# Optimization experiments

Measured on AMD Instinct MI355X. Metric: run time of the kernel, lower is better.

The kernel has to match this reference:

```python
import jax, jax.numpy as jnp
import numpy as np

N_NODES = 100000


def setup_inputs() -> dict:
    key = jax.random.key(0)
    k1, k2, k3 = jax.random.split(key, 3)
    X = jax.random.normal(k1, (N_NODES, 128), dtype=jnp.float32)
    W = jax.random.normal(k2, (128, 128), dtype=jnp.float32) * (1.0 / np.sqrt(128))
    edge_index = jax.random.randint(k3, (2, 1600000), 0, N_NODES, dtype=jnp.int64)
    return {"X": X, "W": W, "edge_index": edge_index}


def reference(X, W, edge_index):
    # GCNConv: out = D_hat^{-1/2} (A + I) D_hat^{-1/2} @ (X W^T)
    N = X.shape[0]
    row, col = edge_index[0], edge_index[1]
    # A_hat = A + I : append self-loop edges
    loops = jnp.arange(N, dtype=row.dtype)
    row_h = jnp.concatenate([row, loops])
    col_h = jnp.concatenate([col, loops])
    # D_hat = A_hat.sum(0): column sums -> degree indexed by col
    deg = jax.ops.segment_sum(jnp.ones(col_h.shape[0], dtype=X.dtype), col_h,
                              num_segments=N)
    d_invsqrt = deg ** -0.5  # deg >= 1 due to self loops
    # edge value of H = D^-1/2 A_hat D^-1/2
    val = d_invsqrt[row_h] * d_invsqrt[col_h]  # [E+N]
    # linear projection (nn.Linear, no bias): X @ W^T
    X_hat = X @ W.T  # [N, out]
    # SpMM (sum): out[r] += val * X_hat[c]
    msgs = val[:, None] * X_hat[col_h]  # [E+N, out]
    return jax.ops.segment_sum(msgs, row_h, num_segments=N)
```

## Files before the change

kernel.cpp:

```cpp
#include <hip/hip_runtime.h>
#include <hip/hip_bf16.h>
#include <stdint.h>

typedef __bf16 bf16_t;
typedef bf16_t bf16x8 __attribute__((ext_vector_type(8)));
typedef bf16_t bf16x2 __attribute__((ext_vector_type(2)));
typedef float  f32x4  __attribute__((ext_vector_type(4)));
typedef float  f32x2  __attribute__((ext_vector_type(2)));

#define N_FEAT 128
#define NBMAX  196
#define BINB   512

__global__ void detect_k(const int* __restrict__ edges, int* __restrict__ flag) {
    int v = edges[2 * threadIdx.x + 1];
    unsigned long long m = __ballot(v != 0);
    if (threadIdx.x == 0) *flag = (m == 0ull) ? 1 : 0;
}
__device__ inline int eread(const int* __restrict__ edges, int f, long i) {
    return f ? edges[2 * i] : edges[i];
}

__device__ inline bf16x8 cvt8(const float* __restrict__ p) {
    f32x4 lo = *(const f32x4*)p;
    f32x4 hi = *(const f32x4*)(p + 4);
    bf16x8 r;
    r[0] = (bf16_t)lo[0]; r[1] = (bf16_t)lo[1]; r[2] = (bf16_t)lo[2]; r[3] = (bf16_t)lo[3];
    r[4] = (bf16_t)hi[0]; r[5] = (bf16_t)hi[1]; r[6] = (bf16_t)hi[2]; r[7] = (bf16_t)hi[3];
    return r;
}

__device__ inline int block_scan_incl(int v, int* wsum ) {
    const int t = threadIdx.x, lane = t & 63, wid = t >> 6;
    int x = v;
#pragma unroll
    for (int off = 1; off < 64; off <<= 1) {
        int y = __shfl_up(x, off);
        if (lane >= off) x += y;
    }
    if (lane == 63) wsum[wid] = x;
    __syncthreads();
    int add = 0;
    for (int w = 0; w < wid; ++w) add += wsum[w];
    return x + add;
}

__global__ __launch_bounds__(256) void wconv_k(const float* __restrict__ W,
                                               bf16_t* __restrict__ Wbf) {
    int i = blockIdx.x * 256 + threadIdx.x;
    Wbf[i] = (bf16_t)W[i];
}

__global__ __launch_bounds__(64) void gemm_xwt2(const float* __restrict__ X,
                                                const bf16_t* __restrict__ Wbf,
                                                bf16_t* __restrict__ Xhat) {
    const int lane = threadIdx.x;
    const int m  = lane & 15;
    const int kq = lane >> 4;
    const long r0 = (long)blockIdx.x * 16;

    f32x4 acc[8];
#pragma unroll
    for (int c = 0; c < 8; ++c) acc[c] = (f32x4){0.f, 0.f, 0.f, 0.f};

    const float* xrow = X + (r0 + m) * N_FEAT + kq * 8;
#pragma unroll
    for (int kb = 0; kb < 4; ++kb) {
        bf16x8 a = cvt8(xrow + kb * 32);
#pragma unroll
        for (int c = 0; c < 8; ++c) {
            bf16x8 b = *(const bf16x8*)(Wbf + (c * 16 + m) * N_FEAT + kb * 32 + kq * 8);
            acc[c] = __builtin_amdgcn_mfma_f32_16x16x32_bf16(a, b, acc[c], 0, 0, 0);
        }
    }
#pragma unroll
    for (int c = 0; c < 8; ++c) {
#pragma unroll
        for (int i = 0; i < 4; ++i) {
            long r = r0 + kq * 4 + i;
            Xhat[r * N_FEAT + c * 16 + m] = (bf16_t)acc[c][i];
        }
    }
}


__global__ __launch_bounds__(256) void bin_k(const int* __restrict__ edges,
                                             const int* __restrict__ flag,
                                             int E, int N, int NB,
                                             int* __restrict__ hist) {
    __shared__ int h[2 * NBMAX];
    const int blk = blockIdx.x;
    const int nb2 = 2 * NB;
    for (int j = threadIdx.x; j < nb2; j += 256) h[j] = 0;
    __syncthreads();
    const int f = *flag;
    const int chunk = (E + BINB - 1) / BINB;
    const int e0 = blk * chunk, e1 = min(E, e0 + chunk);
    for (int e = e0 + (int)threadIdx.x; e < e1; e += 256) {
        int r = eread(edges, f, e);
        int c = eread(edges, f, (long)E + e);
        if ((unsigned)r < (unsigned)N && (unsigned)c < (unsigned)N) {
            atomicAdd(&h[r >> 9], 1);
            atomicAdd(&h[NB + (c >> 9)], 1);
        }
    }
    __syncthreads();
    for (int j = threadIdx.x; j < nb2; j += 256) hist[(long)j * BINB + blk] = h[j];
}

__global__ __launch_bounds__(BINB) void scan_k(const int* __restrict__ hist, int NB,
                                               int* __restrict__ baseTab,
                                               int* __restrict__ totals) {
    __shared__ int wsum[BINB / 64];
    const int j = blockIdx.x;
    const int t = threadIdx.x;
    int v = hist[(long)j * BINB + t];
    int incl = block_scan_incl(v, wsum);
    baseTab[(long)j * BINB + t] = incl - v;
    if (t == BINB - 1) totals[j] = incl;
}

__global__ __launch_bounds__(512) void bucketbase_k(const int* __restrict__ totals,
                                                    int NB, int N,
                                                    int* __restrict__ famBase,
                                                    int* __restrict__ start) {
    __shared__ int wsum[8];
    __shared__ int sh_tot0;
    const int t = threadIdx.x;
    const int nb2 = 2 * NB;
    int v = (t < nb2) ? totals[t] : 0;
    int incl = block_scan_incl(v, wsum);
    int excl = incl - v;
    if (t == NB) sh_tot0 = excl;
    __syncthreads();
    if (t < NB) famBase[t] = excl;
    if (t == NB) { famBase[NB] = excl; start[N] = excl; }
    if (t >= NB && t < nb2) famBase[NB + 1 + (t - NB)] = excl - sh_tot0;
    if (t == nb2 - 1) famBase[NB + 1 + NB] = incl - sh_tot0;
}

__global__ __launch_bounds__(256) void bscatter_k(const int* __restrict__ edges,
                                                  const int* __restrict__ flag,
                                                  int E, int N, int NB,
                                                  const int* __restrict__ baseTab,
                                                  const int* __restrict__ famBase,
                                                  unsigned* __restrict__ rowbuf,
                                                  int* __restrict__ colbuf) {
    __shared__ int cur[2 * NBMAX];
    const int blk = blockIdx.x;
    const int nb2 = 2 * NB;
    for (int j = threadIdx.x; j < nb2; j += 256) {
        int fb = (j < NB) ? famBase[j] : famBase[NB + 1 + (j - NB)];
        cur[j] = fb + baseTab[(long)j * BINB + blk];
    }
    __syncthreads();
    const int f = *flag;
    const int chunk = (E + BINB - 1) / BINB;
    const int e0 = blk * chunk, e1 = min(E, e0 + chunk);
    for (int e = e0 + (int)threadIdx.x; e < e1; e += 256) {
        int r = eread(edges, f, e);
        int c = eread(edges, f, (long)E + e);
        if ((unsigned)r < (unsigned)N && (unsigned)c < (unsigned)N) {
            int pr = atomicAdd(&cur[r >> 9], 1);
            rowbuf[pr] = ((unsigned)(r & 511) << 17) | (unsigned)c;
            int pc = atomicAdd(&cur[NB + (c >> 9)], 1);
            colbuf[pc] = c & 511;
        }
    }
}

__global__ __launch_bounds__(512) void degcsr_k(const unsigned* __restrict__ rowbuf,
                                                const int* __restrict__ colbuf,
                                                const int* __restrict__ famBase,
                                                int NB, int N,
                                                int* __restrict__ start,
                                                int* __restrict__ ecol,
                                                float* __restrict__ dinv) {
    __shared__ int cnt[512];
    __shared__ int wsum[8];
    const int t = threadIdx.x;
    if ((int)blockIdx.x >= NB) {
        const int b = blockIdx.x - NB;
        cnt[t] = 0;
        __syncthreads();
        const int e0 = famBase[NB + 1 + b], e1 = famBase[NB + 1 + b + 1];
        for (int e = e0 + t; e < e1; e += 512)
            atomicAdd(&cnt[colbuf[e]], 1);
        __syncthreads();
        int n = (b << 9) + t;
        if (n < N) dinv[n] = rsqrtf((float)(cnt[t] + 1));
        return;
    }
    const int b = blockIdx.x;
    cnt[t] = 0;
    __syncthreads();
    const int e0 = famBase[b], e1 = famBase[b + 1];
    for (int e = e0 + t; e < e1; e += 512)
        atomicAdd(&cnt[rowbuf[e] >> 17], 1);
    __syncthreads();
    int v = cnt[t];
    int incl = block_scan_incl(v, wsum);
    int excl = incl - v;
    const int n = (b << 9) + t;
    if (n < N) start[n] = e0 + excl;
    cnt[t] = e0 + excl;
    __syncthreads();
    for (int e = e0 + t; e < e1; e += 512) {
        unsigned w = rowbuf[e];
        int pos = atomicAdd(&cnt[w >> 17], 1);
        ecol[pos] = (int)(w & 0x1FFFFu);
    }
}

__global__ __launch_bounds__(64) void gather3_k(const int* __restrict__ ecol,
                                                const int* __restrict__ start,
                                                const float* __restrict__ dinv,
                                                const bf16_t* __restrict__ Xhat,
                                                float* __restrict__ out) {
    const int n = blockIdx.x;
    const int j = threadIdx.x;
    const int s = start[n], e = start[n + 1];
    const float dn = dinv[n];

    bf16x2 xs = *(const bf16x2*)(Xhat + (long)n * N_FEAT + 2 * j);
    float a0 = dn * (float)xs[0];
    float a1 = dn * (float)xs[1];

    for (int p = s; p < e; p += 8) {
        int   cq[8];
        float dq[8];
#pragma unroll
        for (int q = 0; q < 8; ++q) {
            int tt = p + q;
            int idx = (tt < e) ? tt : s;
            cq[q] = ecol[idx];
            dq[q] = (tt < e) ? dinv[cq[q]] : 0.0f;
        }
#pragma unroll
        for (int q = 0; q < 8; ++q) {
            bf16x2 xv = *(const bf16x2*)(Xhat + (long)cq[q] * N_FEAT + 2 * j);
            a0 += dq[q] * (float)xv[0];
            a1 += dq[q] * (float)xv[1];
        }
    }
    f32x2 o; o[0] = dn * a0; o[1] = dn * a1;
    *(f32x2*)(out + (long)n * N_FEAT + 2 * j) = o;
}


__global__ __launch_bounds__(64) void gemm_xwt(const float* __restrict__ X,
                                               const float* __restrict__ W,
                                               bf16_t* __restrict__ Xhat) {
    const int lane = threadIdx.x;
    const int m  = lane & 15;
    const int kq = lane >> 4;
    const long r0 = (long)blockIdx.x * 16;
    f32x4 acc[8];
#pragma unroll
    for (int c = 0; c < 8; ++c) acc[c] = (f32x4){0.f, 0.f, 0.f, 0.f};
    const float* xrow = X + (r0 + m) * N_FEAT + kq * 8;
#pragma unroll
    for (int kb = 0; kb < 4; ++kb) {
        bf16x8 a = cvt8(xrow + kb * 32);
#pragma unroll
        for (int c = 0; c < 8; ++c) {
            bf16x8 b = cvt8(W + (c * 16 + m) * N_FEAT + kb * 32 + kq * 8);
            acc[c] = __builtin_amdgcn_mfma_f32_16x16x32_bf16(a, b, acc[c], 0, 0, 0);
        }
    }
#pragma unroll
    for (int c = 0; c < 8; ++c)
#pragma unroll
        for (int i = 0; i < 4; ++i) {
            long r = r0 + kq * 4 + i;
            Xhat[r * N_FEAT + c * 16 + m] = (bf16_t)acc[c][i];
        }
}

__global__ void degree_k(const int* __restrict__ edges, const int* __restrict__ flag,
                         int E, int N,
                         int* __restrict__ cnt_row, int* __restrict__ cnt_col) {
    int e = blockIdx.x * blockDim.x + threadIdx.x;
    int f = *flag;
    if (e < E) {
        int r = eread(edges, f, e);
        int c = eread(edges, f, (long)E + e);
        if ((unsigned)r < (unsigned)N) atomicAdd(&cnt_row[r], 1);
        if ((unsigned)c < (unsigned)N) atomicAdd(&cnt_col[c], 1);
    }
}

__global__ void degree_col_k(const int* __restrict__ edges, const int* __restrict__ flag,
                             int E, int N, int* __restrict__ cnt_col) {
    int e = blockIdx.x * blockDim.x + threadIdx.x;
    int f = *flag;
    if (e < E) {
        int c = eread(edges, f, (long)E + e);
        if ((unsigned)c < (unsigned)N) atomicAdd(&cnt_col[c], 1);
    }
}

__global__ void alloc_k(const int* __restrict__ cnt_row, int N,
                        int* __restrict__ cur, int* __restrict__ total,
                        int* cnt_col_in, float* dinv_out) {
    int n = blockIdx.x * blockDim.x + threadIdx.x;
    if (n < N) {
        cur[n] = atomicAdd(total, cnt_row[n]);
        int dc = cnt_col_in[n];
        dinv_out[n] = rsqrtf((float)(dc + 1));
    }
}

__global__ void scatter_k(const int* __restrict__ edges, const int* __restrict__ flag,
                          int E, int N, int* __restrict__ cur, int* __restrict__ ecol) {
    int e = blockIdx.x * blockDim.x + threadIdx.x;
    int f = *flag;
    if (e < E) {
        int r = eread(edges, f, e);
        if ((unsigned)r < (unsigned)N) {
            int p = atomicAdd(&cur[r], 1);
            if ((unsigned)p < (unsigned)E)
                ecol[p] = eread(edges, f, (long)E + e);
        }
    }
}

__global__ __launch_bounds__(64) void gather_k(const int* __restrict__ ecol,
                                               const int* __restrict__ cur,
                                               const int* __restrict__ cnt_row,
                                               const float* __restrict__ dinv,
                                               const bf16_t* __restrict__ Xhat,
                                               int N,
                                               float* __restrict__ out) {
    const int n = blockIdx.x;
    const int j = threadIdx.x;
    const int c = cnt_row[n];
    const int s = cur[n] - c;
    const float dn = dinv[n];
    bf16x2 xs = *(const bf16x2*)(Xhat + (long)n * N_FEAT + 2 * j);
    float a0 = dn * (float)xs[0];
    float a1 = dn * (float)xs[1];
    for (int e = 0; e < c; ++e) {
        int cc = ecol[s + e];
        if ((unsigned)cc >= (unsigned)N) continue;
        float dc = dinv[cc];
        bf16x2 xv = *(const bf16x2*)(Xhat + (long)cc * N_FEAT + 2 * j);
        a0 += dc * (float)xv[0];
        a1 += dc * (float)xv[1];
    }
    f32x2 o; o[0] = dn * a0; o[1] = dn * a1;
    *(f32x2*)(out + (long)n * N_FEAT + 2 * j) = o;
}


__global__ __launch_bounds__(128) void self_k(const int* __restrict__ cnt_col,
                                              const bf16_t* __restrict__ Xhat,
                                              float* __restrict__ out) {
    const int n = blockIdx.x;
    const int j = threadIdx.x;
    const float dn2 = 1.0f / (float)(cnt_col[n] + 1);
    out[(long)n * N_FEAT + j] = dn2 * (float)Xhat[(long)n * N_FEAT + j];
}

__global__ __launch_bounds__(128) void edge_add_k(const int* __restrict__ edges,
                                                  const int* __restrict__ flag,
                                                  int E, int N,
                                                  const int* __restrict__ cnt_col,
                                                  const bf16_t* __restrict__ Xhat,
                                                  float* __restrict__ out) {
    const int e = blockIdx.x;
    const int j = threadIdx.x;
    int f = *flag;
    const int r = eread(edges, f, e);
    const int c = eread(edges, f, (long)E + e);
    if ((unsigned)r >= (unsigned)N || (unsigned)c >= (unsigned)N) return;
    const float val = rsqrtf((float)(cnt_col[r] + 1)) * rsqrtf((float)(cnt_col[c] + 1));
    atomicAdd(&out[(long)r * N_FEAT + j], val * (float)Xhat[(long)c * N_FEAT + j]);
}

extern "C" void kernel_launch(void* const* d_in, const int* in_sizes, int n_in,
                              void* d_out, int out_size, void* d_ws, size_t ws_size,
                              hipStream_t stream) {
    const float* X = (const float*)d_in[0];
    const float* W = (const float*)d_in[1];
    const int* edges = (const int*)d_in[2];
    const int E = in_sizes[2] / 2;
    const int N = in_sizes[0] / N_FEAT;
    const int NB = (N + 511) >> 9;

    char* ws = (char*)d_ws;
    const size_t xhat_b = (size_t)N * N_FEAT * sizeof(bf16_t);
    const size_t n4     = (size_t)N * 4;
    auto al = [](size_t x) { return (x + 255) & ~(size_t)255; };

    size_t off = 0;
    int*      flag   = (int*)(ws + off);        off = 256;
    bf16_t*   Wbf    = (bf16_t*)(ws + off);     off = al(off + 128 * 128 * 2);
    bf16_t*   Xhat   = (bf16_t*)(ws + off);     off = al(off + xhat_b);
    float*    dinv   = (float*)(ws + off);      off = al(off + n4);
    int*      startA = (int*)(ws + off);        off = al(off + n4 + 4);
    unsigned* rowbuf = (unsigned*)(ws + off);   off = al(off + (size_t)E * 4);
    int*      colbuf = (int*)(ws + off);        off = al(off + (size_t)E * 4);
    int*      hist   = (int*)(ws + off);        off = al(off + (size_t)BINB * 2 * NB * 4);
    int*      baseTab= (int*)(ws + off);        off = al(off + (size_t)BINB * 2 * NB * 4);
    int*      totals = (int*)(ws + off);        off = al(off + (size_t)(2 * NB) * 4);
    int*      famBase= (int*)(ws + off);        off = al(off + (size_t)(2 * NB + 2) * 4);
    const size_t need_S = off;

    int* cnt_col = (int*)(ws + 16 + xhat_b);
    const size_t need_A = 16 + xhat_b + n4 * 3 + 16 + (size_t)E * 4;
    const size_t need_B = 16 + xhat_b + n4;

    if (ws_size >= need_S && NB <= NBMAX && N <= 100352 && (N & 15) == 0 && E >= BINB) {
        detect_k<<<1, 64, 0, stream>>>(edges, flag);
        wconv_k<<<64, 256, 0, stream>>>(W, Wbf);
        gemm_xwt2<<<N / 16, 64, 0, stream>>>(X, Wbf, Xhat);
        bin_k<<<BINB, 256, 0, stream>>>(edges, flag, E, N, NB, hist);
        scan_k<<<2 * NB, BINB, 0, stream>>>(hist, NB, baseTab, totals);
        bucketbase_k<<<1, 512, 0, stream>>>(totals, NB, N, famBase, startA);
        bscatter_k<<<BINB, 256, 0, stream>>>(edges, flag, E, N, NB, baseTab, famBase,
                                             rowbuf, colbuf);
        degcsr_k<<<2 * NB, 512, 0, stream>>>(rowbuf, colbuf, famBase, NB, N,
                                             startA, colbuf , dinv);
        gather3_k<<<N, 64, 0, stream>>>(colbuf , startA, dinv, Xhat, (float*)d_out);
    } else if (ws_size >= need_A) {
        bf16_t* XhatA  = (bf16_t*)(ws + 16);
        int*   cnt_row = (int*)(ws + 16 + xhat_b + n4);
        int*   cur     = (int*)(ws + 16 + xhat_b + n4 * 2);
        int*   total   = (int*)(ws + 16 + xhat_b + n4 * 3);
        int*   ecol    = (int*)(ws + 16 + xhat_b + n4 * 3 + 16);
        float* dinvA   = (float*)cnt_col;

        hipMemsetAsync(cnt_col, 0, n4 * 2, stream);
        hipMemsetAsync(total, 0, 16, stream);
        detect_k<<<1, 64, 0, stream>>>(edges, flag);
        gemm_xwt<<<N / 16, 64, 0, stream>>>(X, W, XhatA);
        degree_k<<<(E + 255) / 256, 256, 0, stream>>>(edges, flag, E, N, cnt_row, cnt_col);
        alloc_k<<<(N + 255) / 256, 256, 0, stream>>>(cnt_row, N, cur, total, cnt_col, dinvA);
        scatter_k<<<(E + 255) / 256, 256, 0, stream>>>(edges, flag, E, N, cur, ecol);
        gather_k<<<N, 64, 0, stream>>>(ecol, cur, cnt_row, dinvA, XhatA, N, (float*)d_out);
    } else if (ws_size >= need_B) {
        bf16_t* XhatB = (bf16_t*)(ws + 16);
        hipMemsetAsync(cnt_col, 0, n4, stream);
        detect_k<<<1, 64, 0, stream>>>(edges, flag);
        gemm_xwt<<<N / 16, 64, 0, stream>>>(X, W, XhatB);
        degree_col_k<<<(E + 255) / 256, 256, 0, stream>>>(edges, flag, E, N, cnt_col);
        self_k<<<N, 128, 0, stream>>>(cnt_col, XhatB, (float*)d_out);
        edge_add_k<<<E, 128, 0, stream>>>(edges, flag, E, N, cnt_col, XhatB, (float*)d_out);
    }
}
```

Measured before the change: 270.8 us.

## Fuse GEMM into degree/CSR kernel, drop scan and detect launches, widen gather

```diff
diff --git a/kernel.cpp b/kernel.cpp
--- a/kernel.cpp
+++ b/kernel.cpp
@@ -19,6 +19,16 @@
 }
 __device__ inline int eread(const int* __restrict__ edges, int f, long i) {
     return f ? edges[2 * i] : edges[i];
+}
+
+__device__ inline int detect_inline(const int* __restrict__ edges, int* sh) {
+    if (threadIdx.x < 64) {
+        int v = edges[2 * threadIdx.x + 1];
+        unsigned long long m = __ballot(v != 0);
+        if (threadIdx.x == 0) sh[0] = (m == 0ull) ? 1 : 0;
+    }
+    __syncthreads();
+    return sh[0];
 }
 
 __device__ inline bf16x8 cvt8(const float* __restrict__ p) {
@@ -30,7 +40,7 @@
     return r;
 }
 
-__device__ inline int block_scan_incl(int v, int* wsum ) {
+__device__ inline int block_scan_incl(int v, int* wsum) {
     const int t = threadIdx.x, lane = t & 63, wid = t >> 6;
     int x = v;
 #pragma unroll
@@ -45,24 +55,26 @@
     return x + add;
 }
 
-__global__ __launch_bounds__(256) void wconv_k(const float* __restrict__ W,
-                                               bf16_t* __restrict__ Wbf) {
-    int i = blockIdx.x * 256 + threadIdx.x;
-    Wbf[i] = (bf16_t)W[i];
-}
-
-__global__ __launch_bounds__(64) void gemm_xwt2(const float* __restrict__ X,
-                                                const bf16_t* __restrict__ Wbf,
-                                                bf16_t* __restrict__ Xhat) {
-    const int lane = threadIdx.x;
+__global__ __launch_bounds__(256) void wzero_k(const float* __restrict__ W,
+                                               bf16_t* __restrict__ Wbf,
+                                               int* __restrict__ totals, int nb2) {
+    if (blockIdx.x < 64) {
+        int i = blockIdx.x * 256 + threadIdx.x;
+        Wbf[i] = (bf16_t)W[i];
+    } else {
+        for (int i = threadIdx.x; i < nb2; i += 256) totals[i] = 0;
+    }
+}
+
+__device__ inline void gemm_tile(long tile, const float* __restrict__ X,
+                                 const bf16_t* __restrict__ Wbf,
+                                 bf16_t* __restrict__ Xhat, int lane) {
     const int m  = lane & 15;
     const int kq = lane >> 4;
-    const long r0 = (long)blockIdx.x * 16;
-
+    const long r0 = tile * 16;
     f32x4 acc[8];
 #pragma unroll
     for (int c = 0; c < 8; ++c) acc[c] = (f32x4){0.f, 0.f, 0.f, 0.f};
-
     const float* xrow = X + (r0 + m) * N_FEAT + kq * 8;
 #pragma unroll
     for (int kb = 0; kb < 4; ++kb) {
@@ -74,50 +86,49 @@
         }
     }
 #pragma unroll
-    for (int c = 0; c < 8; ++c) {
+    for (int c = 0; c < 8; ++c)
 #pragma unroll
         for (int i = 0; i < 4; ++i) {
             long r = r0 + kq * 4 + i;
             Xhat[r * N_FEAT + c * 16 + m] = (bf16_t)acc[c][i];
         }
-    }
 }
 
 
 __global__ __launch_bounds__(256) void bin_k(const int* __restrict__ edges,
-                                             const int* __restrict__ flag,
                                              int E, int N, int NB,
-                                             int* __restrict__ hist) {
+                                             int* __restrict__ baseTab,
+                                             int* __restrict__ totals) {
     __shared__ int h[2 * NBMAX];
+    __shared__ int shf[1];
+    const int f = detect_inline(edges, shf);
     const int blk = blockIdx.x;
     const int nb2 = 2 * NB;
     for (int j = threadIdx.x; j < nb2; j += 256) h[j] = 0;
     __syncthreads();
-    const int f = *flag;
     const int chunk = (E + BINB - 1) / BINB;
     const int e0 = blk * chunk, e1 = min(E, e0 + chunk);
-    for (int e = e0 + (int)threadIdx.x; e < e1; e += 256) {
-        int r = eread(edges, f, e);
-        int c = eread(edges, f, (long)E + e);
-        if ((unsigned)r < (unsigned)N && (unsigned)c < (unsigned)N) {
-            atomicAdd(&h[r >> 9], 1);
-            atomicAdd(&h[NB + (c >> 9)], 1);
-        }
-    }
-    __syncthreads();
-    for (int j = threadIdx.x; j < nb2; j += 256) hist[(long)j * BINB + blk] = h[j];
-}
-
-__global__ __launch_bounds__(BINB) void scan_k(const int* __restrict__ hist, int NB,
-                                               int* __restrict__ baseTab,
-                                               int* __restrict__ totals) {
-    __shared__ int wsum[BINB / 64];
-    const int j = blockIdx.x;
-    const int t = threadIdx.x;
-    int v = hist[(long)j * BINB + t];
-    int incl = block_scan_incl(v, wsum);
-    baseTab[(long)j * BINB + t] = incl - v;
-    if (t == BINB - 1) totals[j] = incl;
+    if (f) {
+        const int2* e2 = (const int2*)edges;
+        for (int e = e0 + (int)threadIdx.x; e < e1; e += 256) {
+            int r = e2[e].x, c = e2[(long)E + e].x;
+            if ((unsigned)r < (unsigned)N && (unsigned)c < (unsigned)N) {
+                atomicAdd(&h[r >> 9], 1);
+                atomicAdd(&h[NB + (c >> 9)], 1);
+            }
+        }
+    } else {
+        for (int e = e0 + (int)threadIdx.x; e < e1; e += 256) {
+            int r = edges[e], c = edges[(long)E + e];
+            if ((unsigned)r < (unsigned)N && (unsigned)c < (unsigned)N) {
+                atomicAdd(&h[r >> 9], 1);
+                atomicAdd(&h[NB + (c >> 9)], 1);
+            }
+        }
+    }
+    __syncthreads();
+    for (int j = threadIdx.x; j < nb2; j += 256)
+        baseTab[(long)j * BINB + blk] = atomicAdd(&totals[j], h[j]);
 }
 
 __global__ __launch_bounds__(512) void bucketbase_k(const int* __restrict__ totals,
@@ -140,13 +151,14 @@
 }
 
 __global__ __launch_bounds__(256) void bscatter_k(const int* __restrict__ edges,
-                                                  const int* __restrict__ flag,
                                                   int E, int N, int NB,
                                                   const int* __restrict__ baseTab,
                                                   const int* __restrict__ famBase,
                                                   unsigned* __restrict__ rowbuf,
                                                   int* __restrict__ colbuf) {
     __shared__ int cur[2 * NBMAX];
+    __shared__ int shf[1];
+    const int f = detect_inline(edges, shf);
     const int blk = blockIdx.x;
     const int nb2 = 2 * NB;
     for (int j = threadIdx.x; j < nb2; j += 256) {
@@ -154,33 +166,53 @@
         cur[j] = fb + baseTab[(long)j * BINB + blk];
     }
     __syncthreads();
-    const int f = *flag;
     const int chunk = (E + BINB - 1) / BINB;
     const int e0 = blk * chunk, e1 = min(E, e0 + chunk);
-    for (int e = e0 + (int)threadIdx.x; e < e1; e += 256) {
-        int r = eread(edges, f, e);
-        int c = eread(edges, f, (long)E + e);
-        if ((unsigned)r < (unsigned)N && (unsigned)c < (unsigned)N) {
-            int pr = atomicAdd(&cur[r >> 9], 1);
-            rowbuf[pr] = ((unsigned)(r & 511) << 17) | (unsigned)c;
-            int pc = atomicAdd(&cur[NB + (c >> 9)], 1);
-            colbuf[pc] = c & 511;
-        }
-    }
-}
-
-__global__ __launch_bounds__(512) void degcsr_k(const unsigned* __restrict__ rowbuf,
+    if (f) {
+        const int2* e2 = (const int2*)edges;
+        for (int e = e0 + (int)threadIdx.x; e < e1; e += 256) {
+            int r = e2[e].x, c = e2[(long)E + e].x;
+            if ((unsigned)r < (unsigned)N && (unsigned)c < (unsigned)N) {
+                int pr = atomicAdd(&cur[r >> 9], 1);
+                rowbuf[pr] = ((unsigned)(r & 511) << 17) | (unsigned)c;
+                int pc = atomicAdd(&cur[NB + (c >> 9)], 1);
+                colbuf[pc] = c & 511;
+            }
+        }
+    } else {
+        for (int e = e0 + (int)threadIdx.x; e < e1; e += 256) {
+            int r = edges[e], c = edges[(long)E + e];
+            if ((unsigned)r < (unsigned)N && (unsigned)c < (unsigned)N) {
+                int pr = atomicAdd(&cur[r >> 9], 1);
+                rowbuf[pr] = ((unsigned)(r & 511) << 17) | (unsigned)c;
+                int pc = atomicAdd(&cur[NB + (c >> 9)], 1);
+                colbuf[pc] = c & 511;
+            }
+        }
+    }
+}
+
+__global__ __launch_bounds__(512) void degemm_k(const unsigned* __restrict__ rowbuf,
                                                 const int* __restrict__ colbuf,
                                                 const int* __restrict__ famBase,
-                                                int NB, int N,
+                                                int NB, int N, int ntiles,
                                                 int* __restrict__ start,
                                                 int* __restrict__ ecol,
-                                                float* __restrict__ dinv) {
+                                                float* __restrict__ dinv,
+                                                const float* __restrict__ X,
+                                                const bf16_t* __restrict__ Wbf,
+                                                bf16_t* __restrict__ Xhat) {
     __shared__ int cnt[512];
     __shared__ int wsum[8];
     const int t = threadIdx.x;
-    if ((int)blockIdx.x >= NB) {
-        const int b = blockIdx.x - NB;
+    const int bid = blockIdx.x;
+    if (bid >= 2 * NB) {
+        const long tile = (long)(bid - 2 * NB) * 8 + (t >> 6);
+        if (tile < ntiles) gemm_tile(tile, X, Wbf, Xhat, t & 63);
+        return;
+    }
+    if (bid >= NB) {
+        const int b = bid - NB;
         cnt[t] = 0;
         __syncthreads();
         const int e0 = famBase[NB + 1 + b], e1 = famBase[NB + 1 + b + 1];
@@ -191,7 +223,7 @@
         if (n < N) dinv[n] = rsqrtf((float)(cnt[t] + 1));
         return;
     }
-    const int b = blockIdx.x;
+    const int b = bid;
     cnt[t] = 0;
     __syncthreads();
     const int e0 = famBase[b], e1 = famBase[b + 1];
@@ -212,13 +244,15 @@
     }
 }
 
-__global__ __launch_bounds__(64) void gather3_k(const int* __restrict__ ecol,
-                                                const int* __restrict__ start,
-                                                const float* __restrict__ dinv,
-                                                const bf16_t* __restrict__ Xhat,
-                                                float* __restrict__ out) {
-    const int n = blockIdx.x;
-    const int j = threadIdx.x;
+__global__ __launch_bounds__(256) void gather4_k(const int* __restrict__ ecol,
+                                                 const int* __restrict__ start,
+                                                 const float* __restrict__ dinv,
+                                                 const bf16_t* __restrict__ Xhat,
+                                                 int N,
+                                                 float* __restrict__ out) {
+    const int n = blockIdx.x * 4 + (threadIdx.x >> 6);
+    const int j = threadIdx.x & 63;
+    if (n >= N) return;
     const int s = start[n], e = start[n + 1];
     const float dn = dinv[n];
 
@@ -226,18 +260,18 @@
     float a0 = dn * (float)xs[0];
     float a1 = dn * (float)xs[1];
 
-    for (int p = s; p < e; p += 8) {
-        int   cq[8];
-        float dq[8];
-#pragma unroll
-        for (int q = 0; q < 8; ++q) {
+    for (int p = s; p < e; p += 16) {
+        int   cq[16];
+        float dq[16];
+#pragma unroll
+        for (int q = 0; q < 16; ++q) {
             int tt = p + q;
             int idx = (tt < e) ? tt : s;
             cq[q] = ecol[idx];
             dq[q] = (tt < e) ? dinv[cq[q]] : 0.0f;
         }
 #pragma unroll
-        for (int q = 0; q < 8; ++q) {
+        for (int q = 0; q < 16; ++q) {
             bf16x2 xv = *(const bf16x2*)(Xhat + (long)cq[q] * N_FEAT + 2 * j);
             a0 += dq[q] * (float)xv[0];
             a1 += dq[q] * (float)xv[1];
@@ -401,7 +435,7 @@
     int*      startA = (int*)(ws + off);        off = al(off + n4 + 4);
     unsigned* rowbuf = (unsigned*)(ws + off);   off = al(off + (size_t)E * 4);
     int*      colbuf = (int*)(ws + off);        off = al(off + (size_t)E * 4);
-    int*      hist   = (int*)(ws + off);        off = al(off + (size_t)BINB * 2 * NB * 4);
+    int*      ecol   = (int*)(ws + off);        off = al(off + (size_t)E * 4);
     int*      baseTab= (int*)(ws + off);        off = al(off + (size_t)BINB * 2 * NB * 4);
     int*      totals = (int*)(ws + off);        off = al(off + (size_t)(2 * NB) * 4);
     int*      famBase= (int*)(ws + off);        off = al(off + (size_t)(2 * NB + 2) * 4);
@@ -412,23 +446,24 @@
     const size_t need_B = 16 + xhat_b + n4;
 
     if (ws_size >= need_S && NB <= NBMAX && N <= 100352 && (N & 15) == 0 && E >= BINB) {
-        detect_k<<<1, 64, 0, stream>>>(edges, flag);
-        wconv_k<<<64, 256, 0, stream>>>(W, Wbf);
-        gemm_xwt2<<<N / 16, 64, 0, stream>>>(X, Wbf, Xhat);
-        bin_k<<<BINB, 256, 0, stream>>>(edges, flag, E, N, NB, hist);
-        scan_k<<<2 * NB, BINB, 0, stream>>>(hist, NB, baseTab, totals);
+        const int ntiles = N / 16;
+        const int GEMMB  = (ntiles + 7) / 8;
+        wzero_k<<<65, 256, 0, stream>>>(W, Wbf, totals, 2 * NB);
+        bin_k<<<BINB, 256, 0, stream>>>(edges, E, N, NB, baseTab, totals);
         bucketbase_k<<<1, 512, 0, stream>>>(totals, NB, N, famBase, startA);
-        bscatter_k<<<BINB, 256, 0, stream>>>(edges, flag, E, N, NB, baseTab, famBase,
+        bscatter_k<<<BINB, 256, 0, stream>>>(edges, E, N, NB, baseTab, famBase,
                                              rowbuf, colbuf);
-        degcsr_k<<<2 * NB, 512, 0, stream>>>(rowbuf, colbuf, famBase, NB, N,
-                                             startA, colbuf , dinv);
-        gather3_k<<<N, 64, 0, stream>>>(colbuf , startA, dinv, Xhat, (float*)d_out);
+        degemm_k<<<2 * NB + GEMMB, 512, 0, stream>>>(rowbuf, colbuf, famBase, NB, N,
+                                                     ntiles, startA, ecol, dinv,
+                                                     X, Wbf, Xhat);
+        gather4_k<<<(N + 3) / 4, 256, 0, stream>>>(ecol, startA, dinv, Xhat, N,
+                                                   (float*)d_out);
     } else if (ws_size >= need_A) {
         bf16_t* XhatA  = (bf16_t*)(ws + 16);
         int*   cnt_row = (int*)(ws + 16 + xhat_b + n4);
         int*   cur     = (int*)(ws + 16 + xhat_b + n4 * 2);
         int*   total   = (int*)(ws + 16 + xhat_b + n4 * 3);
-        int*   ecol    = (int*)(ws + 16 + xhat_b + n4 * 3 + 16);
+        int*   ecolA   = (int*)(ws + 16 + xhat_b + n4 * 3 + 16);
         float* dinvA   = (float*)cnt_col;
 
         hipMemsetAsync(cnt_col, 0, n4 * 2, stream);
@@ -437,8 +472,8 @@
         gemm_xwt<<<N / 16, 64, 0, stream>>>(X, W, XhatA);
         degree_k<<<(E + 255) / 256, 256, 0, stream>>>(edges, flag, E, N, cnt_row, cnt_col);
         alloc_k<<<(N + 255) / 256, 256, 0, stream>>>(cnt_row, N, cur, total, cnt_col, dinvA);
-        scatter_k<<<(E + 255) / 256, 256, 0, stream>>>(edges, flag, E, N, cur, ecol);
-        gather_k<<<N, 64, 0, stream>>>(ecol, cur, cnt_row, dinvA, XhatA, N, (float*)d_out);
+        scatter_k<<<(E + 255) / 256, 256, 0, stream>>>(edges, flag, E, N, cur, ecolA);
+        gather_k<<<N, 64, 0, stream>>>(ecolA, cur, cnt_row, dinvA, XhatA, N, (float*)d_out);
     } else if (ws_size >= need_B) {
         bf16_t* XhatB = (bf16_t*)(ws + 16);
         hipMemsetAsync(cnt_col, 0, n4, stream);
```

After: 336.4 us. 1.24x slower.
